# Kernel tuning notes

Measured on AMD Instinct MI355X. Metric: run time of the kernel, lower is better.

## Reference

```python
import jax, jax.numpy as jnp
import numpy as np

B, S, D_MODEL = 2, 2048, 2048
N_HEADS, N_KV = 16, 4
HEAD_DIM = D_MODEL // N_HEADS  # 128
N_REP = N_HEADS // N_KV        # 4


def _apply_rope(x, cos, sin):
    # x: [B, H, S, Dh]; cos/sin: [S, Dh//2]
    c = cos[None, None, :, :]
    s = sin[None, None, :, :]
    x_even = x[..., ::2]
    x_odd = x[..., 1::2]
    re = x_even * c - x_odd * s
    ro = x_even * s + x_odd * c
    # interleave back: stack on last axis then flatten -> [..., Dh]
    return jnp.stack([re, ro], axis=-1).reshape(x.shape)


def setup_inputs() -> dict:
    key = jax.random.key(0)
    ks = jax.random.split(key, 7)
    std = 1.0 / np.sqrt(D_MODEL)
    return {
        "x": jax.random.normal(ks[0], (B, S, D_MODEL), dtype=jnp.float32),
        "rope_cos": jax.random.uniform(ks[1], (S, HEAD_DIM // 2), dtype=jnp.float32),
        "rope_sin": jax.random.uniform(ks[2], (S, HEAD_DIM // 2), dtype=jnp.float32),
        "Wq": jax.random.normal(ks[3], (D_MODEL, N_HEADS * HEAD_DIM), dtype=jnp.float32) * std,
        "Wk": jax.random.normal(ks[4], (D_MODEL, N_KV * HEAD_DIM), dtype=jnp.float32) * std,
        "Wv": jax.random.normal(ks[5], (D_MODEL, N_KV * HEAD_DIM), dtype=jnp.float32) * std,
        "Wo": jax.random.normal(ks[6], (N_HEADS * HEAD_DIM, D_MODEL), dtype=jnp.float32) * std,
    }


def reference(x, rope_cos, rope_sin, Wq, Wk, Wv, Wo):
    batch, seq_len, _ = x.shape
    q = (x @ Wq).reshape(batch, seq_len, N_HEADS, HEAD_DIM).transpose(0, 2, 1, 3)
    k = (x @ Wk).reshape(batch, seq_len, N_KV, HEAD_DIM).transpose(0, 2, 1, 3)
    v = (x @ Wv).reshape(batch, seq_len, N_KV, HEAD_DIM).transpose(0, 2, 1, 3)

    q = _apply_rope(q, rope_cos[:seq_len], rope_sin[:seq_len])
    k = _apply_rope(k, rope_cos[:seq_len], rope_sin[:seq_len])

    # GQA: group q heads by kv head instead of materializing repeated k/v.
    qg = q.reshape(batch, N_KV, N_REP, seq_len, HEAD_DIM)
    scale = 1.0 / np.sqrt(HEAD_DIM)
    scores = jnp.einsum('bgrqd,bgkd->bgrqk', qg, k) * scale

    causal = jnp.tril(jnp.ones((seq_len, seq_len), dtype=bool))
    scores = jnp.where(causal[None, None, None, :, :], scores, -jnp.inf)
    weights = jax.nn.softmax(scores, axis=-1)

    out = jnp.einsum('bgrqk,bgkd->bgrqd', weights, v)
    out = out.reshape(batch, N_HEADS, seq_len, HEAD_DIM).transpose(0, 2, 1, 3)
    out = out.reshape(batch, seq_len, N_HEADS * HEAD_DIM)
    return out @ Wo
```

## Files before the change

### kernel.cpp

```cpp
#include <hip/hip_runtime.h>
#include <hip/hip_bf16.h>
#include <math.h>

typedef __bf16 bf16x8_t __attribute__((ext_vector_type(8)));
typedef float f32x4 __attribute__((ext_vector_type(4)));
typedef unsigned short ushort8 __attribute__((ext_vector_type(8)));

__device__ inline unsigned short f2bf(float f) {
  unsigned int u = __builtin_bit_cast(unsigned int, f);
  u += 0x7fffu + ((u >> 16) & 1u);
  return (unsigned short)(u >> 16);
}
__device__ inline float b2f(unsigned short s) {
  unsigned int u = ((unsigned int)s) << 16;
  return __builtin_bit_cast(float, u);
}
__device__ inline unsigned int pack2bf(float lo, float hi) {
  return (unsigned int)f2bf(lo) | ((unsigned int)f2bf(hi) << 16);
}

__device__ __forceinline__ void gll16(const void* g, void* l) {
  __builtin_amdgcn_global_load_lds((const __attribute__((address_space(1))) void*)g,
                                   (__attribute__((address_space(3))) void*)l, 16, 0, 0);
}

__global__ void cvt_k(const float* __restrict__ X, unsigned short* __restrict__ Xb, int total8) {
  int i = blockIdx.x * blockDim.x + threadIdx.x;
  if (i >= total8) return;
  const float4* p = (const float4*)X + 2 * (size_t)i;
  float4 a = p[0], b = p[1];
  ushort8 v;
  v[0] = f2bf(a.x); v[1] = f2bf(a.y); v[2] = f2bf(a.z); v[3] = f2bf(a.w);
  v[4] = f2bf(b.x); v[5] = f2bf(b.y); v[6] = f2bf(b.z); v[7] = f2bf(b.w);
  ((ushort8*)Xb)[i] = v;
}

__global__ void twc_k(const float* __restrict__ W, unsigned short* __restrict__ Wt, int K, int N) {
  __shared__ float tile[32][33];
  int k0 = blockIdx.x * 32, n0 = blockIdx.y * 32;
  int tx = threadIdx.x, ty = threadIdx.y;
#pragma unroll
  for (int i = 0; i < 32; i += 8) tile[ty + i][tx] = W[(size_t)(k0 + ty + i) * N + n0 + tx];
  __syncthreads();
#pragma unroll
  for (int i = 0; i < 32; i += 8)
    Wt[(size_t)(n0 + ty + i) * K + k0 + tx] = f2bf(tile[tx][ty + i]);
}

template <bool OUT_BF16>
__global__ __launch_bounds__(256) void gemm_tn(const unsigned short* __restrict__ A,
                                               const unsigned short* __restrict__ Bt,
                                               void* __restrict__ Cv, int M, int N, int K) {
  __shared__ __align__(16) unsigned short As[128 * 32];
  __shared__ __align__(16) unsigned short Bs[128 * 32];
  const int t = threadIdx.x, w = t >> 6, lane = t & 63;
  const int la = lane & 15, lk = lane >> 4;
  const int wr = w >> 1, wc = w & 1;
  const int bm = blockIdx.y * 128, bn = blockIdx.x * 128;
  const int lrow = lane >> 2, lcb = (lane & 3) * 8;

  f32x4 acc[4][4] = {};

  for (int k0 = 0; k0 < K; k0 += 32) {
#pragma unroll
    for (int u = 0; u < 2; ++u) {
      int c = w * 2 + u;
      gll16(A + (size_t)(bm + c * 16 + lrow) * K + k0 + lcb, (char*)As + c * 1024);
      gll16(Bt + (size_t)(bn + c * 16 + lrow) * K + k0 + lcb, (char*)Bs + c * 1024);
    }
    __syncthreads();

    bf16x8_t a[4], b[4];
#pragma unroll
    for (int m = 0; m < 4; ++m)
      a[m] = __builtin_bit_cast(bf16x8_t,
                                *(const ushort8*)(As + (wr * 64 + m * 16 + la) * 32 + lk * 8));
#pragma unroll
    for (int n = 0; n < 4; ++n)
      b[n] = __builtin_bit_cast(bf16x8_t,
                                *(const ushort8*)(Bs + (wc * 64 + n * 16 + la) * 32 + lk * 8));
#pragma unroll
    for (int m = 0; m < 4; ++m)
#pragma unroll
      for (int n = 0; n < 4; ++n)
        acc[m][n] = __builtin_amdgcn_mfma_f32_16x16x32_bf16(a[m], b[n], acc[m][n], 0, 0, 0);
    __syncthreads();
  }

#pragma unroll
  for (int m = 0; m < 4; ++m) {
#pragma unroll
    for (int n = 0; n < 4; ++n) {
#pragma unroll
      for (int r = 0; r < 4; ++r) {
        int row = bm + wr * 64 + m * 16 + lk * 4 + r;
        int col = bn + wc * 64 + n * 16 + la;
        if (OUT_BF16)
          ((unsigned short*)Cv)[(size_t)row * N + col] = f2bf(acc[m][n][r]);
        else
          ((float*)Cv)[(size_t)row * N + col] = acc[m][n][r];
      }
    }
  }
}

__global__ void rope_k(unsigned short* X, const float* __restrict__ cs,
                       const float* __restrict__ sn, int log2ppr, int rowlen, int total) {
  int idx = blockIdx.x * blockDim.x + threadIdx.x;
  if (idx >= total) return;
  int row = idx >> log2ppr;
  int p = idx & ((1 << log2ppr) - 1);
  int h = p >> 6, i = p & 63;
  int s = row & 2047;
  float c = cs[s * 64 + i], sv = sn[s * 64 + i];
  unsigned short* base = X + (size_t)row * rowlen + h * 128 + 2 * i;
  float e = b2f(base[0]), o = b2f(base[1]);
  base[0] = f2bf(e * c - o * sv);
  base[1] = f2bf(e * sv + o * c);
}

__global__ void transpose_v(const unsigned short* __restrict__ QKV, unsigned short* __restrict__ Vt) {
  __shared__ unsigned short tile[32][33];
  int bg = blockIdx.z;
  int b = bg >> 2, g = bg & 3;
  int s0 = blockIdx.x * 32, d0 = blockIdx.y * 32;
  int tx = threadIdx.x, ty = threadIdx.y;
#pragma unroll
  for (int i = 0; i < 32; i += 8)
    tile[ty + i][tx] = QKV[((size_t)(b * 2048 + s0 + ty + i)) * 3072 + 2560 + g * 128 + d0 + tx];
  __syncthreads();
#pragma unroll
  for (int i = 0; i < 32; i += 8)
    Vt[((size_t)(bg * 128 + d0 + ty + i)) * 2048 + s0 + tx] = tile[tx][ty + i];
}

__global__ __launch_bounds__(256, 2) void attn_mfma(const unsigned short* __restrict__ QKV,
                                                    const unsigned short* __restrict__ Vt,
                                                    unsigned short* __restrict__ Ob) {
  const int S = 2048;
  __shared__ __align__(16) unsigned short Ks[2][64 * 128];
  __shared__ __align__(16) unsigned short Vs[2][128 * 64];
  __shared__ __align__(16) unsigned short Ps[4 * 32 * 64];

  const int t = threadIdx.x;
  const int w = t >> 6, lane = t & 63;
  const int la = lane & 15, lk = lane >> 4;
  const int b = blockIdx.z, h = blockIdx.y, g = h >> 2;
  const int qt = (b == 0) ? (gridDim.x - 1 - blockIdx.x) : blockIdx.x;
  const int q0 = qt * 128;
  const int qw = q0 + w * 32;
  const float scale = 0.08838834764831845f;

  const unsigned short* ksrc[4];
  const unsigned short* vsrc[4];
#pragma unroll
  for (int u = 0; u < 4; ++u) {
    int kr = 16 * w + 4 * u + (lane >> 4);
    int kp = lane & 15;
    ksrc[u] = QKV + (size_t)(b * S + kr) * 3072 + 2048 + g * 128 + (kp ^ (kr & 7)) * 8;
    int vr = 32 * w + 8 * u + (lane >> 3);
    int vp = lane & 7;
    vsrc[u] = Vt + (size_t)((b * 4 + g) * 128 + vr) * 2048 + (vp ^ (vr & 7)) * 8;
  }

  bf16x8_t qf[2][4];
#pragma unroll
  for (int qi = 0; qi < 2; ++qi)
#pragma unroll
    for (int dt = 0; dt < 4; ++dt)
      qf[qi][dt] = __builtin_bit_cast(
          bf16x8_t, *(const ushort8*)(QKV + (size_t)(b * S + qw + qi * 16 + la) * 3072 + h * 128 +
                                      dt * 32 + lk * 8));

  f32x4 oa[2][8];
#pragma unroll
  for (int qi = 0; qi < 2; ++qi)
#pragma unroll
    for (int dt = 0; dt < 8; ++dt) oa[qi][dt] = (f32x4){0.f, 0.f, 0.f, 0.f};
  float mr[2] = {-1e30f, -1e30f}, lr[2] = {0.f, 0.f};

  const int n_kt = 2 * qt + 2;
  const int kmask0 = qw & ~63;
  char* pw = (char*)Ps + w * 4096;

#pragma unroll
  for (int u = 0; u < 4; ++u) {
    gll16(ksrc[u], (char*)Ks[0] + (4 * w + u) * 1024);
    gll16(vsrc[u], (char*)Vs[0] + (4 * w + u) * 1024);
  }
  __syncthreads();

  int cur = 0;
  for (int kt = 0; kt < n_kt; ++kt) {
    const int k0 = kt * 64;
    if (kt + 1 < n_kt) {
      const int kn = k0 + 64;
#pragma unroll
      for (int u = 0; u < 4; ++u) {
        gll16(ksrc[u] + (size_t)kn * 3072, (char*)Ks[cur ^ 1] + (4 * w + u) * 1024);
        gll16(vsrc[u] + kn, (char*)Vs[cur ^ 1] + (4 * w + u) * 1024);
      }
    }

    if (k0 <= qw + 31) {
      char* Ksb = (char*)Ks[cur];
      char* Vsb = (char*)Vs[cur];

      f32x4 sacc[2][4];
#pragma unroll
      for (int qi = 0; qi < 2; ++qi)
#pragma unroll
        for (int ktc = 0; ktc < 4; ++ktc) sacc[qi][ktc] = (f32x4){0.f, 0.f, 0.f, 0.f};
      __builtin_amdgcn_s_setprio(1);
#pragma unroll
      for (int ktc = 0; ktc < 4; ++ktc) {
        int row = ktc * 16 + la;
#pragma unroll
        for (int dt = 0; dt < 4; ++dt) {
          bf16x8_t kf = __builtin_bit_cast(
              bf16x8_t, *(const ushort8*)(Ksb + row * 256 + ((((dt << 2) + lk) ^ (row & 7)) << 4)));
          sacc[0][ktc] = __builtin_amdgcn_mfma_f32_16x16x32_bf16(kf, qf[0][dt], sacc[0][ktc], 0, 0, 0);
          sacc[1][ktc] = __builtin_amdgcn_mfma_f32_16x16x32_bf16(kf, qf[1][dt], sacc[1][ktc], 0, 0, 0);
        }
      }
      __builtin_amdgcn_s_setprio(0);

      const bool domask = (k0 == kmask0);
#pragma unroll
      for (int qi = 0; qi < 2; ++qi) {
        const int q = qw + qi * 16 + la;
        float p[4][4];
        float tm = -1e30f;
#pragma unroll
        for (int ktc = 0; ktc < 4; ++ktc)
#pragma unroll
          for (int r = 0; r < 4; ++r) {
            float sv = sacc[qi][ktc][r] * scale;
            if (domask && (k0 + ktc * 16 + lk * 4 + r > q)) sv = -1e30f;
            p[ktc][r] = sv;
            tm = fmaxf(tm, sv);
          }
        tm = fmaxf(tm, __shfl_xor(tm, 16));
        tm = fmaxf(tm, __shfl_xor(tm, 32));
        float mn;
        if (__all(tm - mr[qi] <= 8.f)) {
          mn = mr[qi];
        } else {
          mn = fmaxf(mr[qi], tm);
          float sc = __expf(mr[qi] - mn);
          mr[qi] = mn;
          lr[qi] *= sc;
          float scb[4];
#pragma unroll
          for (int r = 0; r < 4; ++r) scb[r] = __shfl(sc, lk * 4 + r);
#pragma unroll
          for (int dt = 0; dt < 8; ++dt)
#pragma unroll
            for (int r = 0; r < 4; ++r) oa[qi][dt][r] *= scb[r];
        }
        float ts = 0.f;
#pragma unroll
        for (int ktc = 0; ktc < 4; ++ktc)
#pragma unroll
          for (int r = 0; r < 4; ++r) {
            float e = __expf(p[ktc][r] - mn);
            p[ktc][r] = e;
            ts += e;
          }
        ts += __shfl_xor(ts, 16);
        ts += __shfl_xor(ts, 32);
        lr[qi] += ts;
        char* pq = pw + (qi * 16 + la) * 128;
#pragma unroll
        for (int ktc = 0; ktc < 4; ++ktc) {
          uint2 gv;
          gv.x = pack2bf(p[ktc][0], p[ktc][1]);
          gv.y = pack2bf(p[ktc][2], p[ktc][3]);
          *(uint2*)(pq + ((32 * ktc + 8 * lk) ^ ((la & 7) << 4))) = gv;
        }
      }
      asm volatile("s_waitcnt lgkmcnt(0)" ::: "memory");

      bf16x8_t pf[2][2];
#pragma unroll
      for (int qi = 0; qi < 2; ++qi)
#pragma unroll
        for (int ks = 0; ks < 2; ++ks)
          pf[qi][ks] = __builtin_bit_cast(
              bf16x8_t, *(const ushort8*)(pw + (qi * 16 + la) * 128 +
                                          ((64 * ks + 16 * lk) ^ ((la & 7) << 4))));
      __builtin_amdgcn_s_setprio(1);
#pragma unroll
      for (int dt = 0; dt < 8; ++dt) {
        int d = dt * 16 + la;
#pragma unroll
        for (int ks = 0; ks < 2; ++ks) {
          bf16x8_t vf = __builtin_bit_cast(
              bf16x8_t, *(const ushort8*)(Vsb + d * 128 + ((((ks << 2) + lk) ^ (d & 7)) << 4)));
          oa[0][dt] = __builtin_amdgcn_mfma_f32_16x16x32_bf16(pf[0][ks], vf, oa[0][dt], 0, 0, 0);
          oa[1][dt] = __builtin_amdgcn_mfma_f32_16x16x32_bf16(pf[1][ks], vf, oa[1][dt], 0, 0, 0);
        }
      }
      __builtin_amdgcn_s_setprio(0);
    }

    __syncthreads();
    cur ^= 1;
  }

#pragma unroll
  for (int qi = 0; qi < 2; ++qi) {
    float inv = 1.f / lr[qi];
    float invb[4];
#pragma unroll
    for (int r = 0; r < 4; ++r) invb[r] = __shfl(inv, lk * 4 + r);
#pragma unroll
    for (int dt = 0; dt < 8; ++dt)
#pragma unroll
      for (int r = 0; r < 4; ++r)
        Ob[(size_t)(b * S + qw + qi * 16 + lk * 4 + r) * 2048 + h * 128 + dt * 16 + la] =
            f2bf(oa[qi][dt][r] * invb[r]);
  }
}

extern "C" void kernel_launch(void* const* d_in, const int* in_sizes, int n_in,
                              void* d_out, int out_size, void* d_ws, size_t ws_size,
                              hipStream_t stream) {
  const float* x = (const float*)d_in[0];
  const float* rc = (const float*)d_in[1];
  const float* rs = (const float*)d_in[2];
  const float* Wq = (const float*)d_in[3];
  const float* Wk = (const float*)d_in[4];
  const float* Wv = (const float*)d_in[5];
  const float* Wo = (const float*)d_in[6];
  float* out = (float*)d_out;

  const int B = 2, S = 2048, DM = 2048;
  const int M = B * S;

  unsigned short* xb = (unsigned short*)d_ws;
  unsigned short* QKV = xb + (size_t)M * DM;
  unsigned short* WallT = QKV + (size_t)M * 3072;
  unsigned short* WoT = WallT;
  unsigned short* Vt = WallT + (size_t)2048 * 2048;
  unsigned short* Ob = xb;

  dim3 blk(256);

  cvt_k<<<(M * DM / 8 + 255) / 256, blk, 0, stream>>>(x, xb, M * DM / 8);
  twc_k<<<dim3(64, 64), dim3(32, 8), 0, stream>>>(Wq, WallT, DM, DM);
  twc_k<<<dim3(64, 16), dim3(32, 8), 0, stream>>>(Wk, WallT + (size_t)2048 * DM, DM, 512);
  twc_k<<<dim3(64, 16), dim3(32, 8), 0, stream>>>(Wv, WallT + (size_t)2560 * DM, DM, 512);

  gemm_tn<true><<<dim3(3072 / 128, M / 128), blk, 0, stream>>>(xb, WallT, QKV, M, 3072, DM);

  twc_k<<<dim3(64, 64), dim3(32, 8), 0, stream>>>(Wo, WoT, DM, DM);

  int totq = M * 1024;
  rope_k<<<(totq + 255) / 256, blk, 0, stream>>>(QKV, rc, rs, 10, 3072, totq);
  int totk = M * 256;
  rope_k<<<(totk + 255) / 256, blk, 0, stream>>>(QKV + 2048, rc, rs, 8, 3072, totk);

  transpose_v<<<dim3(S / 32, 4, B * 4), dim3(32, 8), 0, stream>>>(QKV, Vt);

  attn_mfma<<<dim3(S / 128, 16, B), dim3(256), 0, stream>>>(QKV, Vt, Ob);

  gemm_tn<false><<<dim3(DM / 128, M / 128), blk, 0, stream>>>(Ob, WoT, out, M, DM, DM);
}
```

Baseline: 250.0 us.

## Fuse RoPE into QKV GEMM epilogue and pair causal q-tiles in 512-thread attention

Applies RoPE inside the QKV projection GEMM epilogue using a lane shuffle to fetch the even/odd partner, which removes the two separate rope passes over Q and K. Restructures attention to 512-thread blocks covering 256 queries, with each block processing two q-tiles (a and 7-a) in sequence so the causal work per block is balanced. Each block of eight waves shares its K/V tile loads, at the cost of more LDS and a larger block.

```diff
diff --git a/kernel.cpp b/kernel.cpp
--- a/kernel.cpp
+++ b/kernel.cpp
@@ -47,10 +47,12 @@
     Wt[(size_t)(n0 + ty + i) * K + k0 + tx] = f2bf(tile[tx][ty + i]);
 }
 
-template <bool OUT_BF16>
+template <bool OUT_BF16, bool ROPE>
 __global__ __launch_bounds__(256) void gemm_tn(const unsigned short* __restrict__ A,
                                                const unsigned short* __restrict__ Bt,
-                                               void* __restrict__ Cv, int M, int N, int K) {
+                                               void* __restrict__ Cv, int M, int N, int K,
+                                               const float* __restrict__ cs,
+                                               const float* __restrict__ sn, int ropeLim) {
   __shared__ __align__(16) unsigned short As[128 * 32];
   __shared__ __align__(16) unsigned short Bs[128 * 32];
   const int t = threadIdx.x, w = t >> 6, lane = t & 63;
@@ -91,32 +93,28 @@
   for (int m = 0; m < 4; ++m) {
 #pragma unroll
     for (int n = 0; n < 4; ++n) {
+      const int col = bn + wc * 64 + n * 16 + la;
+      const bool doRope = ROPE && (col < ropeLim);
 #pragma unroll
       for (int r = 0; r < 4; ++r) {
         int row = bm + wr * 64 + m * 16 + lk * 4 + r;
-        int col = bn + wc * 64 + n * 16 + la;
+        float val = acc[m][n][r];
+        if (ROPE) {
+          float pval = __shfl_xor(val, 1);
+          if (doRope) {
+            int srow = row & 2047;
+            int i = (col & 127) >> 1;
+            float cc = cs[srow * 64 + i], ss = sn[srow * 64 + i];
+            val = (la & 1) ? (pval * ss + val * cc) : (val * cc - pval * ss);
+          }
+        }
         if (OUT_BF16)
-          ((unsigned short*)Cv)[(size_t)row * N + col] = f2bf(acc[m][n][r]);
+          ((unsigned short*)Cv)[(size_t)row * N + col] = f2bf(val);
         else
-          ((float*)Cv)[(size_t)row * N + col] = acc[m][n][r];
+          ((float*)Cv)[(size_t)row * N + col] = val;
       }
     }
   }
-}
-
-__global__ void rope_k(unsigned short* X, const float* __restrict__ cs,
-                       const float* __restrict__ sn, int log2ppr, int rowlen, int total) {
-  int idx = blockIdx.x * blockDim.x + threadIdx.x;
-  if (idx >= total) return;
-  int row = idx >> log2ppr;
-  int p = idx & ((1 << log2ppr) - 1);
-  int h = p >> 6, i = p & 63;
-  int s = row & 2047;
-  float c = cs[s * 64 + i], sv = sn[s * 64 + i];
-  unsigned short* base = X + (size_t)row * rowlen + h * 128 + 2 * i;
-  float e = b2f(base[0]), o = b2f(base[1]);
-  base[0] = f2bf(e * c - o * sv);
-  base[1] = f2bf(e * sv + o * c);
 }
 
 __global__ void transpose_v(const unsigned short* __restrict__ QKV, unsigned short* __restrict__ Vt) {
@@ -134,192 +132,197 @@
     Vt[((size_t)(bg * 128 + d0 + ty + i)) * 2048 + s0 + tx] = tile[tx][ty + i];
 }
 
-__global__ __launch_bounds__(256, 2) void attn_mfma(const unsigned short* __restrict__ QKV,
+__global__ __launch_bounds__(512, 2) void attn_mfma(const unsigned short* __restrict__ QKV,
                                                     const unsigned short* __restrict__ Vt,
                                                     unsigned short* __restrict__ Ob) {
   const int S = 2048;
   __shared__ __align__(16) unsigned short Ks[2][64 * 128];
   __shared__ __align__(16) unsigned short Vs[2][128 * 64];
-  __shared__ __align__(16) unsigned short Ps[4 * 32 * 64];
+  __shared__ __align__(16) unsigned short Ps[8 * 32 * 64];
 
   const int t = threadIdx.x;
   const int w = t >> 6, lane = t & 63;
   const int la = lane & 15, lk = lane >> 4;
   const int b = blockIdx.z, h = blockIdx.y, g = h >> 2;
-  const int qt = (b == 0) ? (gridDim.x - 1 - blockIdx.x) : blockIdx.x;
-  const int q0 = qt * 128;
-  const int qw = q0 + w * 32;
+  const int a = blockIdx.x;
   const float scale = 0.08838834764831845f;
 
-  const unsigned short* ksrc[4];
-  const unsigned short* vsrc[4];
-#pragma unroll
-  for (int u = 0; u < 4; ++u) {
-    int kr = 16 * w + 4 * u + (lane >> 4);
+  const unsigned short* ksrc[2];
+  const unsigned short* vsrc[2];
+#pragma unroll
+  for (int u = 0; u < 2; ++u) {
+    int kr = 8 * w + 4 * u + (lane >> 4);
     int kp = lane & 15;
     ksrc[u] = QKV + (size_t)(b * S + kr) * 3072 + 2048 + g * 128 + (kp ^ (kr & 7)) * 8;
-    int vr = 32 * w + 8 * u + (lane >> 3);
+    int vr = 16 * w + 8 * u + (lane >> 3);
     int vp = lane & 7;
     vsrc[u] = Vt + (size_t)((b * 4 + g) * 128 + vr) * 2048 + (vp ^ (vr & 7)) * 8;
   }
-
-  bf16x8_t qf[2][4];
-#pragma unroll
-  for (int qi = 0; qi < 2; ++qi)
-#pragma unroll
-    for (int dt = 0; dt < 4; ++dt)
-      qf[qi][dt] = __builtin_bit_cast(
-          bf16x8_t, *(const ushort8*)(QKV + (size_t)(b * S + qw + qi * 16 + la) * 3072 + h * 128 +
-                                      dt * 32 + lk * 8));
-
-  f32x4 oa[2][8];
-#pragma unroll
-  for (int qi = 0; qi < 2; ++qi)
-#pragma unroll
-    for (int dt = 0; dt < 8; ++dt) oa[qi][dt] = (f32x4){0.f, 0.f, 0.f, 0.f};
-  float mr[2] = {-1e30f, -1e30f}, lr[2] = {0.f, 0.f};
-
-  const int n_kt = 2 * qt + 2;
-  const int kmask0 = qw & ~63;
   char* pw = (char*)Ps + w * 4096;
 
-#pragma unroll
-  for (int u = 0; u < 4; ++u) {
-    gll16(ksrc[u], (char*)Ks[0] + (4 * w + u) * 1024);
-    gll16(vsrc[u], (char*)Vs[0] + (4 * w + u) * 1024);
-  }
-  __syncthreads();
-
   int cur = 0;
-  for (int kt = 0; kt < n_kt; ++kt) {
-    const int k0 = kt * 64;
-    if (kt + 1 < n_kt) {
-      const int kn = k0 + 64;
-#pragma unroll
-      for (int u = 0; u < 4; ++u) {
-        gll16(ksrc[u] + (size_t)kn * 3072, (char*)Ks[cur ^ 1] + (4 * w + u) * 1024);
-        gll16(vsrc[u] + kn, (char*)Vs[cur ^ 1] + (4 * w + u) * 1024);
+  for (int pass = 0; pass < 2; ++pass) {
+    const int qt = pass ? (7 - a) : a;
+    const int qw = qt * 256 + w * 32;
+    const int n_kt = 4 * (qt + 1);
+    const int kmask0 = qw & ~63;
+
+    bf16x8_t qf[2][4];
+#pragma unroll
+    for (int qi = 0; qi < 2; ++qi)
+#pragma unroll
+      for (int dt = 0; dt < 4; ++dt)
+        qf[qi][dt] = __builtin_bit_cast(
+            bf16x8_t, *(const ushort8*)(QKV + (size_t)(b * S + qw + qi * 16 + la) * 3072 +
+                                        h * 128 + dt * 32 + lk * 8));
+
+    f32x4 oa[2][8];
+#pragma unroll
+    for (int qi = 0; qi < 2; ++qi)
+#pragma unroll
+      for (int dt = 0; dt < 8; ++dt) oa[qi][dt] = (f32x4){0.f, 0.f, 0.f, 0.f};
+    float mr[2] = {-1e30f, -1e30f}, lr[2] = {0.f, 0.f};
+
+#pragma unroll
+    for (int u = 0; u < 2; ++u) {
+      gll16(ksrc[u], (char*)Ks[cur] + (2 * w + u) * 1024);
+      gll16(vsrc[u], (char*)Vs[cur] + (2 * w + u) * 1024);
+    }
+    __syncthreads();
+
+    for (int kt = 0; kt < n_kt; ++kt) {
+      const int k0 = kt * 64;
+      if (kt + 1 < n_kt) {
+        const int kn = k0 + 64;
+#pragma unroll
+        for (int u = 0; u < 2; ++u) {
+          gll16(ksrc[u] + (size_t)kn * 3072, (char*)Ks[cur ^ 1] + (2 * w + u) * 1024);
+          gll16(vsrc[u] + kn, (char*)Vs[cur ^ 1] + (2 * w + u) * 1024);
+        }
       }
-    }
-
-    if (k0 <= qw + 31) {
-      char* Ksb = (char*)Ks[cur];
-      char* Vsb = (char*)Vs[cur];
-
-      f32x4 sacc[2][4];
-#pragma unroll
-      for (int qi = 0; qi < 2; ++qi)
-#pragma unroll
-        for (int ktc = 0; ktc < 4; ++ktc) sacc[qi][ktc] = (f32x4){0.f, 0.f, 0.f, 0.f};
-      __builtin_amdgcn_s_setprio(1);
-#pragma unroll
-      for (int ktc = 0; ktc < 4; ++ktc) {
-        int row = ktc * 16 + la;
-#pragma unroll
-        for (int dt = 0; dt < 4; ++dt) {
-          bf16x8_t kf = __builtin_bit_cast(
-              bf16x8_t, *(const ushort8*)(Ksb + row * 256 + ((((dt << 2) + lk) ^ (row & 7)) << 4)));
-          sacc[0][ktc] = __builtin_amdgcn_mfma_f32_16x16x32_bf16(kf, qf[0][dt], sacc[0][ktc], 0, 0, 0);
-          sacc[1][ktc] = __builtin_amdgcn_mfma_f32_16x16x32_bf16(kf, qf[1][dt], sacc[1][ktc], 0, 0, 0);
-        }
+
+      if (k0 <= qw + 31) {
+        char* Ksb = (char*)Ks[cur];
+        char* Vsb = (char*)Vs[cur];
+
+        f32x4 sacc[2][4];
+#pragma unroll
+        for (int qi = 0; qi < 2; ++qi)
+#pragma unroll
+          for (int ktc = 0; ktc < 4; ++ktc) sacc[qi][ktc] = (f32x4){0.f, 0.f, 0.f, 0.f};
+        __builtin_amdgcn_s_setprio(1);
+#pragma unroll
+        for (int ktc = 0; ktc < 4; ++ktc) {
+          int row = ktc * 16 + la;
+#pragma unroll
+          for (int dt = 0; dt < 4; ++dt) {
+            bf16x8_t kf = __builtin_bit_cast(
+                bf16x8_t,
+                *(const ushort8*)(Ksb + row * 256 + ((((dt << 2) + lk) ^ (row & 7)) << 4)));
+            sacc[0][ktc] =
+                __builtin_amdgcn_mfma_f32_16x16x32_bf16(kf, qf[0][dt], sacc[0][ktc], 0, 0, 0);
+            sacc[1][ktc] =
+                __builtin_amdgcn_mfma_f32_16x16x32_bf16(kf, qf[1][dt], sacc[1][ktc], 0, 0, 0);
+          }
+        }
+        __builtin_amdgcn_s_setprio(0);
+
+        const bool domask = (k0 == kmask0);
+#pragma unroll
+        for (int qi = 0; qi < 2; ++qi) {
+          const int q = qw + qi * 16 + la;
+          float p[4][4];
+          float tm = -1e30f;
+#pragma unroll
+          for (int ktc = 0; ktc < 4; ++ktc)
+#pragma unroll
+            for (int r = 0; r < 4; ++r) {
+              float sv = sacc[qi][ktc][r] * scale;
+              if (domask && (k0 + ktc * 16 + lk * 4 + r > q)) sv = -1e30f;
+              p[ktc][r] = sv;
+              tm = fmaxf(tm, sv);
+            }
+          tm = fmaxf(tm, __shfl_xor(tm, 16));
+          tm = fmaxf(tm, __shfl_xor(tm, 32));
+          float mn;
+          if (__all(tm - mr[qi] <= 8.f)) {
+            mn = mr[qi];
+          } else {
+            mn = fmaxf(mr[qi], tm);
+            float sc = __expf(mr[qi] - mn);
+            mr[qi] = mn;
+            lr[qi] *= sc;
+            float scb[4];
+#pragma unroll
+            for (int r = 0; r < 4; ++r) scb[r] = __shfl(sc, lk * 4 + r);
+#pragma unroll
+            for (int dt = 0; dt < 8; ++dt)
+#pragma unroll
+              for (int r = 0; r < 4; ++r) oa[qi][dt][r] *= scb[r];
+          }
+          float ts = 0.f;
+#pragma unroll
+          for (int ktc = 0; ktc < 4; ++ktc)
+#pragma unroll
+            for (int r = 0; r < 4; ++r) {
+              float e = __expf(p[ktc][r] - mn);
+              p[ktc][r] = e;
+              ts += e;
+            }
+          ts += __shfl_xor(ts, 16);
+          ts += __shfl_xor(ts, 32);
+          lr[qi] += ts;
+          char* pq = pw + (qi * 16 + la) * 128;
+#pragma unroll
+          for (int ktc = 0; ktc < 4; ++ktc) {
+            uint2 gv;
+            gv.x = pack2bf(p[ktc][0], p[ktc][1]);
+            gv.y = pack2bf(p[ktc][2], p[ktc][3]);
+            *(uint2*)(pq + ((32 * ktc + 8 * lk) ^ ((la & 7) << 4))) = gv;
+          }
+        }
+        asm volatile("s_waitcnt lgkmcnt(0)" ::: "memory");
+
+        bf16x8_t pf[2][2];
+#pragma unroll
+        for (int qi = 0; qi < 2; ++qi)
+#pragma unroll
+          for (int ks = 0; ks < 2; ++ks)
+            pf[qi][ks] = __builtin_bit_cast(
+                bf16x8_t, *(const ushort8*)(pw + (qi * 16 + la) * 128 +
+                                            ((64 * ks + 16 * lk) ^ ((la & 7) << 4))));
+        __builtin_amdgcn_s_setprio(1);
+#pragma unroll
+        for (int dt = 0; dt < 8; ++dt) {
+          int d = dt * 16 + la;
+#pragma unroll
+          for (int ks = 0; ks < 2; ++ks) {
+            bf16x8_t vf = __builtin_bit_cast(
+                bf16x8_t, *(const ushort8*)(Vsb + d * 128 + ((((ks << 2) + lk) ^ (d & 7)) << 4)));
+            oa[0][dt] = __builtin_amdgcn_mfma_f32_16x16x32_bf16(pf[0][ks], vf, oa[0][dt], 0, 0, 0);
+            oa[1][dt] = __builtin_amdgcn_mfma_f32_16x16x32_bf16(pf[1][ks], vf, oa[1][dt], 0, 0, 0);
+          }
+        }
+        __builtin_amdgcn_s_setprio(0);
       }
-      __builtin_amdgcn_s_setprio(0);
-
-      const bool domask = (k0 == kmask0);
-#pragma unroll
-      for (int qi = 0; qi < 2; ++qi) {
-        const int q = qw + qi * 16 + la;
-        float p[4][4];
-        float tm = -1e30f;
-#pragma unroll
-        for (int ktc = 0; ktc < 4; ++ktc)
-#pragma unroll
-          for (int r = 0; r < 4; ++r) {
-            float sv = sacc[qi][ktc][r] * scale;
-            if (domask && (k0 + ktc * 16 + lk * 4 + r > q)) sv = -1e30f;
-            p[ktc][r] = sv;
-            tm = fmaxf(tm, sv);
-          }
-        tm = fmaxf(tm, __shfl_xor(tm, 16));
-        tm = fmaxf(tm, __shfl_xor(tm, 32));
-        float mn;
-        if (__all(tm - mr[qi] <= 8.f)) {
-          mn = mr[qi];
-        } else {
-          mn = fmaxf(mr[qi], tm);
-          float sc = __expf(mr[qi] - mn);
-          mr[qi] = mn;
-          lr[qi] *= sc;
-          float scb[4];
-#pragma unroll
-          for (int r = 0; r < 4; ++r) scb[r] = __shfl(sc, lk * 4 + r);
-#pragma unroll
-          for (int dt = 0; dt < 8; ++dt)
-#pragma unroll
-            for (int r = 0; r < 4; ++r) oa[qi][dt][r] *= scb[r];
-        }
-        float ts = 0.f;
-#pragma unroll
-        for (int ktc = 0; ktc < 4; ++ktc)
-#pragma unroll
-          for (int r = 0; r < 4; ++r) {
-            float e = __expf(p[ktc][r] - mn);
-            p[ktc][r] = e;
-            ts += e;
-          }
-        ts += __shfl_xor(ts, 16);
-        ts += __shfl_xor(ts, 32);
-        lr[qi] += ts;
-        char* pq = pw + (qi * 16 + la) * 128;
-#pragma unroll
-        for (int ktc = 0; ktc < 4; ++ktc) {
-          uint2 gv;
-          gv.x = pack2bf(p[ktc][0], p[ktc][1]);
-          gv.y = pack2bf(p[ktc][2], p[ktc][3]);
-          *(uint2*)(pq + ((32 * ktc + 8 * lk) ^ ((la & 7) << 4))) = gv;
-        }
-      }
-      asm volatile("s_waitcnt lgkmcnt(0)" ::: "memory");
-
-      bf16x8_t pf[2][2];
-#pragma unroll
-      for (int qi = 0; qi < 2; ++qi)
-#pragma unroll
-        for (int ks = 0; ks < 2; ++ks)
-          pf[qi][ks] = __builtin_bit_cast(
-              bf16x8_t, *(const ushort8*)(pw + (qi * 16 + la) * 128 +
-                                          ((64 * ks + 16 * lk) ^ ((la & 7) << 4))));
-      __builtin_amdgcn_s_setprio(1);
-#pragma unroll
-      for (int dt = 0; dt < 8; ++dt) {
-        int d = dt * 16 + la;
-#pragma unroll
-        for (int ks = 0; ks < 2; ++ks) {
-          bf16x8_t vf = __builtin_bit_cast(
-              bf16x8_t, *(const ushort8*)(Vsb + d * 128 + ((((ks << 2) + lk) ^ (d & 7)) << 4)));
-          oa[0][dt] = __builtin_amdgcn_mfma_f32_16x16x32_bf16(pf[0][ks], vf, oa[0][dt], 0, 0, 0);
-          oa[1][dt] = __builtin_amdgcn_mfma_f32_16x16x32_bf16(pf[1][ks], vf, oa[1][dt], 0, 0, 0);
-        }
-      }
-      __builtin_amdgcn_s_setprio(0);
-    }
-
-    __syncthreads();
-    cur ^= 1;
-  }
-
-#pragma unroll
-  for (int qi = 0; qi < 2; ++qi) {
-    float inv = 1.f / lr[qi];
-    float invb[4];
-#pragma unroll
-    for (int r = 0; r < 4; ++r) invb[r] = __shfl(inv, lk * 4 + r);
-#pragma unroll
-    for (int dt = 0; dt < 8; ++dt)
-#pragma unroll
-      for (int r = 0; r < 4; ++r)
-        Ob[(size_t)(b * S + qw + qi * 16 + lk * 4 + r) * 2048 + h * 128 + dt * 16 + la] =
-            f2bf(oa[qi][dt][r] * invb[r]);
+
+      __syncthreads();
+      cur ^= 1;
+    }
+
+#pragma unroll
+    for (int qi = 0; qi < 2; ++qi) {
+      float inv = 1.f / lr[qi];
+      float invb[4];
+#pragma unroll
+      for (int r = 0; r < 4; ++r) invb[r] = __shfl(inv, lk * 4 + r);
+#pragma unroll
+      for (int dt = 0; dt < 8; ++dt)
+#pragma unroll
+        for (int r = 0; r < 4; ++r)
+          Ob[(size_t)(b * S + qw + qi * 16 + lk * 4 + r) * 2048 + h * 128 + dt * 16 + la] =
+              f2bf(oa[qi][dt][r] * invb[r]);
+    }
   }
 }
 
@@ -352,18 +355,15 @@
   twc_k<<<dim3(64, 16), dim3(32, 8), 0, stream>>>(Wk, WallT + (size_t)2048 * DM, DM, 512);
   twc_k<<<dim3(64, 16), dim3(32, 8), 0, stream>>>(Wv, WallT + (size_t)2560 * DM, DM, 512);
 
-  gemm_tn<true><<<dim3(3072 / 128, M / 128), blk, 0, stream>>>(xb, WallT, QKV, M, 3072, DM);
+  gemm_tn<true, true><<<dim3(3072 / 128, M / 128), blk, 0, stream>>>(xb, WallT, QKV, M, 3072, DM,
+                                                                     rc, rs, 2560);
 
   twc_k<<<dim3(64, 64), dim3(32, 8), 0, stream>>>(Wo, WoT, DM, DM);
 
-  int totq = M * 1024;
-  rope_k<<<(totq + 255) / 256, blk, 0, stream>>>(QKV, rc, rs, 10, 3072, totq);
-  int totk = M * 256;
-  rope_k<<<(totk + 255) / 256, blk, 0, stream>>>(QKV + 2048, rc, rs, 8, 3072, totk);
-
   transpose_v<<<dim3(S / 32, 4, B * 4), dim3(32, 8), 0, stream>>>(QKV, Vt);
 
-  attn_mfma<<<dim3(S / 128, 16, B), dim3(256), 0, stream>>>(QKV, Vt, Ob);
-
-  gemm_tn<false><<<dim3(DM / 128, M / 128), blk, 0, stream>>>(Ob, WoT, out, M, DM, DM);
-}
+  attn_mfma<<<dim3(8, 16, B), dim3(512), 0, stream>>>(QKV, Vt, Ob);
+
+  gemm_tn<false, false><<<dim3(DM / 128, M / 128), blk, 0, stream>>>(Ob, WoT, out, M, DM, DM,
+                                                                     nullptr, nullptr, 0);
+}
```

Result: slower. 298.8 us (+19.5%).

## Fuse RoPE into QKV GEMM epilogue and double-buffer GEMM LDS tiles

Applied to the files above, without the earlier changes.

The two standalone RoPE kernels are removed and the rotation is applied in the QKV GEMM epilogue, using a lane shuffle to fetch the even/odd partner value before the bf16 store. The GEMM main loop now double-buffers its LDS tiles so the next K-slice load is issued before the current MFMAs, dropping one barrier per iteration. This removes a read-modify-write pass over Q and K and aims to overlap loads with compute. The cost is twice the LDS per block, which may lower occupancy, plus extra epilogue work for the cos/sin loads and shuffles.

```diff
diff --git a/kernel.cpp b/kernel.cpp
--- a/kernel.cpp
+++ b/kernel.cpp
@@ -47,76 +47,88 @@
     Wt[(size_t)(n0 + ty + i) * K + k0 + tx] = f2bf(tile[tx][ty + i]);
 }
 
-template <bool OUT_BF16>
+template <bool OUT_BF16, bool ROPE>
 __global__ __launch_bounds__(256) void gemm_tn(const unsigned short* __restrict__ A,
                                                const unsigned short* __restrict__ Bt,
-                                               void* __restrict__ Cv, int M, int N, int K) {
-  __shared__ __align__(16) unsigned short As[128 * 32];
-  __shared__ __align__(16) unsigned short Bs[128 * 32];
+                                               void* __restrict__ Cv, int M, int N, int K,
+                                               const float* __restrict__ cs,
+                                               const float* __restrict__ sn, int ropeLim) {
+  __shared__ __align__(16) unsigned short As[2][128 * 32];
+  __shared__ __align__(16) unsigned short Bs[2][128 * 32];
   const int t = threadIdx.x, w = t >> 6, lane = t & 63;
   const int la = lane & 15, lk = lane >> 4;
   const int wr = w >> 1, wc = w & 1;
   const int bm = blockIdx.y * 128, bn = blockIdx.x * 128;
   const int lrow = lane >> 2, lcb = (lane & 3) * 8;
 
+  const unsigned short* Ab = A + (size_t)(bm + (w * 2) * 16 + lrow) * K + lcb;
+  const unsigned short* Ab1 = A + (size_t)(bm + (w * 2 + 1) * 16 + lrow) * K + lcb;
+  const unsigned short* Bb = Bt + (size_t)(bn + (w * 2) * 16 + lrow) * K + lcb;
+  const unsigned short* Bb1 = Bt + (size_t)(bn + (w * 2 + 1) * 16 + lrow) * K + lcb;
+  const int c0 = w * 2, c1 = w * 2 + 1;
+
   f32x4 acc[4][4] = {};
 
-  for (int k0 = 0; k0 < K; k0 += 32) {
-#pragma unroll
-    for (int u = 0; u < 2; ++u) {
-      int c = w * 2 + u;
-      gll16(A + (size_t)(bm + c * 16 + lrow) * K + k0 + lcb, (char*)As + c * 1024);
-      gll16(Bt + (size_t)(bn + c * 16 + lrow) * K + k0 + lcb, (char*)Bs + c * 1024);
+  gll16(Ab, (char*)As[0] + c0 * 1024);
+  gll16(Ab1, (char*)As[0] + c1 * 1024);
+  gll16(Bb, (char*)Bs[0] + c0 * 1024);
+  gll16(Bb1, (char*)Bs[0] + c1 * 1024);
+
+  const int nt = K / 32;
+  int cur = 0;
+  for (int kt = 0; kt < nt; ++kt) {
+    __syncthreads();
+    if (kt + 1 < nt) {
+      const int kn = (kt + 1) * 32;
+      gll16(Ab + kn, (char*)As[cur ^ 1] + c0 * 1024);
+      gll16(Ab1 + kn, (char*)As[cur ^ 1] + c1 * 1024);
+      gll16(Bb + kn, (char*)Bs[cur ^ 1] + c0 * 1024);
+      gll16(Bb1 + kn, (char*)Bs[cur ^ 1] + c1 * 1024);
     }
-    __syncthreads();
 
     bf16x8_t a[4], b[4];
 #pragma unroll
     for (int m = 0; m < 4; ++m)
-      a[m] = __builtin_bit_cast(bf16x8_t,
-                                *(const ushort8*)(As + (wr * 64 + m * 16 + la) * 32 + lk * 8));
+      a[m] = __builtin_bit_cast(
+          bf16x8_t, *(const ushort8*)(As[cur] + (wr * 64 + m * 16 + la) * 32 + lk * 8));
 #pragma unroll
     for (int n = 0; n < 4; ++n)
-      b[n] = __builtin_bit_cast(bf16x8_t,
-                                *(const ushort8*)(Bs + (wc * 64 + n * 16 + la) * 32 + lk * 8));
+      b[n] = __builtin_bit_cast(
+          bf16x8_t, *(const ushort8*)(Bs[cur] + (wc * 64 + n * 16 + la) * 32 + lk * 8));
 #pragma unroll
     for (int m = 0; m < 4; ++m)
 #pragma unroll
       for (int n = 0; n < 4; ++n)
         acc[m][n] = __builtin_amdgcn_mfma_f32_16x16x32_bf16(a[m], b[n], acc[m][n], 0, 0, 0);
-    __syncthreads();
+    cur ^= 1;
   }
 
 #pragma unroll
   for (int m = 0; m < 4; ++m) {
 #pragma unroll
     for (int n = 0; n < 4; ++n) {
+      const int col = bn + wc * 64 + n * 16 + la;
+      const bool doRope = ROPE && (col < ropeLim);
 #pragma unroll
       for (int r = 0; r < 4; ++r) {
         int row = bm + wr * 64 + m * 16 + lk * 4 + r;
-        int col = bn + wc * 64 + n * 16 + la;
+        float val = acc[m][n][r];
+        if (ROPE) {
+          float pval = __shfl_xor(val, 1);
+          if (doRope) {
+            int srow = row & 2047;
+            int i = (col & 127) >> 1;
+            float cc = cs[srow * 64 + i], ss = sn[srow * 64 + i];
+            val = (la & 1) ? (pval * ss + val * cc) : (val * cc - pval * ss);
+          }
+        }
         if (OUT_BF16)
-          ((unsigned short*)Cv)[(size_t)row * N + col] = f2bf(acc[m][n][r]);
+          ((unsigned short*)Cv)[(size_t)row * N + col] = f2bf(val);
         else
-          ((float*)Cv)[(size_t)row * N + col] = acc[m][n][r];
+          ((float*)Cv)[(size_t)row * N + col] = val;
       }
     }
   }
-}
-
-__global__ void rope_k(unsigned short* X, const float* __restrict__ cs,
-                       const float* __restrict__ sn, int log2ppr, int rowlen, int total) {
-  int idx = blockIdx.x * blockDim.x + threadIdx.x;
-  if (idx >= total) return;
-  int row = idx >> log2ppr;
-  int p = idx & ((1 << log2ppr) - 1);
-  int h = p >> 6, i = p & 63;
-  int s = row & 2047;
-  float c = cs[s * 64 + i], sv = sn[s * 64 + i];
-  unsigned short* base = X + (size_t)row * rowlen + h * 128 + 2 * i;
-  float e = b2f(base[0]), o = b2f(base[1]);
-  base[0] = f2bf(e * c - o * sv);
-  base[1] = f2bf(e * sv + o * c);
 }
 
 __global__ void transpose_v(const unsigned short* __restrict__ QKV, unsigned short* __restrict__ Vt) {
@@ -352,18 +364,15 @@
   twc_k<<<dim3(64, 16), dim3(32, 8), 0, stream>>>(Wk, WallT + (size_t)2048 * DM, DM, 512);
   twc_k<<<dim3(64, 16), dim3(32, 8), 0, stream>>>(Wv, WallT + (size_t)2560 * DM, DM, 512);
 
-  gemm_tn<true><<<dim3(3072 / 128, M / 128), blk, 0, stream>>>(xb, WallT, QKV, M, 3072, DM);
+  gemm_tn<true, true><<<dim3(3072 / 128, M / 128), blk, 0, stream>>>(xb, WallT, QKV, M, 3072, DM,
+                                                                     rc, rs, 2560);
 
   twc_k<<<dim3(64, 64), dim3(32, 8), 0, stream>>>(Wo, WoT, DM, DM);
 
-  int totq = M * 1024;
-  rope_k<<<(totq + 255) / 256, blk, 0, stream>>>(QKV, rc, rs, 10, 3072, totq);
-  int totk = M * 256;
-  rope_k<<<(totk + 255) / 256, blk, 0, stream>>>(QKV + 2048, rc, rs, 8, 3072, totk);
-
   transpose_v<<<dim3(S / 32, 4, B * 4), dim3(32, 8), 0, stream>>>(QKV, Vt);
 
   attn_mfma<<<dim3(S / 128, 16, B), dim3(256), 0, stream>>>(QKV, Vt, Ob);
 
-  gemm_tn<false><<<dim3(DM / 128, M / 128), blk, 0, stream>>>(Ob, WoT, out, M, DM, DM);
-}
+  gemm_tn<false, false><<<dim3(DM / 128, M / 128), blk, 0, stream>>>(Ob, WoT, out, M, DM, DM,
+                                                                     nullptr, nullptr, 0);
+}
```

Result: faster. 233.3 us (-6.7%).
